# Performance work log

Measured on AMD Instinct MI355X. Metric: run time of the kernel, lower is better.

Reference implementation:

```python
import jax, jax.numpy as jnp
import numpy as np
import math

SAMPLE_RATE = 16000
CUTOFF = 7500.0
Q = 0.707  # torchaudio default for lowpass_biquad

def _lowpass_biquad_coeffs(sample_rate, cutoff_freq, Q):
    w0 = 2.0 * math.pi * cutoff_freq / sample_rate
    alpha = math.sin(w0) / (2.0 * Q)
    cos_w0 = math.cos(w0)
    b0 = (1.0 - cos_w0) / 2.0
    b1 = 1.0 - cos_w0
    b2 = b0
    a0 = 1.0 + alpha
    a1 = -2.0 * cos_w0
    a2 = 1.0 - alpha
    # normalize by a0 (as torchaudio's biquad/lfilter does)
    return (b0 / a0, b1 / a0, b2 / a0, a1 / a0, a2 / a0)


def setup_inputs() -> dict:
    key = jax.random.key(0)
    x = jax.random.normal(key, (64, 320000), dtype=jnp.float32)
    return {"x": x}


def reference(x) -> jnp.ndarray:
    b0, b1, b2, a1, a2 = _lowpass_biquad_coeffs(SAMPLE_RATE, CUTOFF, Q)
    b0 = jnp.asarray(b0, x.dtype); b1 = jnp.asarray(b1, x.dtype)
    b2 = jnp.asarray(b2, x.dtype); a1 = jnp.asarray(a1, x.dtype)
    a2 = jnp.asarray(a2, x.dtype)

    B = x.shape[0]
    xT = jnp.swapaxes(x, 0, 1)  # [T, B] -> scan over time

    def step(carry, xn):
        x1, x2, y1, y2 = carry  # each [B]
        yn = b0 * xn + b1 * x1 + b2 * x2 - a1 * y1 - a2 * y2
        return (xn, x1, yn, y1), yn

    z = jnp.zeros((B,), x.dtype)
    _, yT = jax.lax.scan(step, (z, z, z, z), xT)
    return jnp.swapaxes(yT, 0, 1)  # [B, T]
```

## Files before the change

kernel.cpp:

```cpp
#include <hip/hip_runtime.h>
#include <cmath>

#ifndef M_PI
#define M_PI 3.14159265358979323846
#endif

constexpr int T_LEN    = 320000;
constexpr int ROW_VECS = T_LEN / 4;
constexpr int B_ROWS   = 64;
constexpr int CHUNK    = 32;
constexpr int VPT      = CHUNK / 4;
constexpr int NCHUNK   = T_LEN / CHUNK;
constexpr int BLK_CHUNKS = 128;
constexpr int BLK_SPAN   = BLK_CHUNKS * CHUNK;
constexpr int HALO       = 3;
constexpr int HALO_VECS  = HALO * VPT;
constexpr int TILE_VECS  = HALO_VECS + BLK_CHUNKS * VPT;

__device__ __forceinline__ int swzv(int V) { return V ^ ((V >> 3) & 7); }

typedef const __attribute__((address_space(1))) void glb_void;
typedef __attribute__((address_space(3))) void lds_void;

__global__ __launch_bounds__(256, 8) void biquad_gll_kernel(
    const float* __restrict__ x, float* __restrict__ y,
    float b0, float b1, float b2, float a1, float a2,
    float q30, float p30, float q31, float p31) {
  const int b    = blockIdx.x;
  const int row  = blockIdx.y;
  const int t    = threadIdx.x;
  const int wave = t >> 6;
  const int lane = t & 63;

  const int S       = b * BLK_SPAN;
  const int nchunks = min(BLK_CHUNKS, (T_LEN - S) / CHUNK);
  const int nvecs   = nchunks * VPT;
  const int ntot    = HALO_VECS + nvecs;

  const float4* xr4 = reinterpret_cast<const float4*>(x + (size_t)row * T_LEN);
  float*        yr  = y + (size_t)row * T_LEN;

  __shared__ float4 tile[TILE_VECS];
  __shared__ float4 st[HALO + BLK_CHUNKS];

  {
    const int gofs = S / 4 - HALO_VECS;
    for (int r = wave; r * 64 < ntot; r += 4) {
      int s  = r * 64 + lane;
      int gv = gofs + swzv(s);
      if (s < ntot && gv >= 0) {
        __builtin_amdgcn_global_load_lds((glb_void*)(xr4 + gv),
                                         (lds_void*)(tile + r * 64), 16, 0, 0);
      }
    }
    if (b == 0 && t < HALO_VECS) tile[t] = make_float4(0.f, 0.f, 0.f, 0.f);
  }
  __syncthreads();

  auto stepf = [&](float xn, float& X1, float& X2, float& Y1, float& Y2) -> float {
    float tt = fmaf(b2, X2, fmaf(b1, X1, b0 * xn));
    float u  = fmaf(-a2, Y2, tt);
    float yn = fmaf(-a1, Y1, u);
    X2 = X1; X1 = xn;
    Y2 = Y1; Y1 = yn;
    return yn;
  };

  if (t < HALO) {
    float4 h[VPT];
#pragma unroll
    for (int k = 0; k < VPT; ++k) h[k] = tile[swzv(t * VPT + k)];
    float hxl1 = h[VPT - 1].w, hxl2 = h[VPT - 1].z;
    float hx1 = 0.f, hx2 = 0.f, hy1 = 0.f, hy2 = 0.f;
#pragma unroll
    for (int k = 0; k < VPT; ++k) {
      stepf(h[k].x, hx1, hx2, hy1, hy2); stepf(h[k].y, hx1, hx2, hy1, hy2);
      stepf(h[k].z, hx1, hx2, hy1, hy2); stepf(h[k].w, hx1, hx2, hy1, hy2);
    }
    st[t] = make_float4(hy1, hy2, hxl1, hxl2);
  }

  const bool active = (t < nchunks);
  float4 m[VPT];
  const int vb = HALO_VECS + t * VPT;
  if (active) {
#pragma unroll
    for (int k = 0; k < VPT; ++k) m[k] = tile[swzv(vb + k)];
    float xl1 = m[VPT - 1].w, xl2 = m[VPT - 1].z;
    float x1 = 0.f, x2 = 0.f, y1 = 0.f, y2 = 0.f;
#pragma unroll
    for (int k = 0; k < VPT; ++k) {
      float4 v = m[k];
      m[k] = make_float4(stepf(v.x, x1, x2, y1, y2), stepf(v.y, x1, x2, y1, y2),
                         stepf(v.z, x1, x2, y1, y2), stepf(v.w, x1, x2, y1, y2));
    }
    st[HALO + t] = make_float4(y1, y2, xl1, xl2);
  }
  __syncthreads();

  if (active) {
    const int i = HALO + t;
    float4 sm3 = st[i - 3], sm2 = st[i - 2], sm1 = st[i - 1];
    float cA0 = fmaf(b1, sm3.z, fmaf(b2, sm3.w, fmaf(-a1, sm3.x, -a2 * sm3.y)));
    float cA1 = fmaf(-a1, cA0, fmaf(b2, sm3.z, -a2 * sm3.x));
    float yA1 = fmaf(q31, cA0, fmaf(p31, cA1, sm2.x));
    float yA2 = fmaf(q30, cA0, fmaf(p30, cA1, sm2.y));
    float cB0 = fmaf(b1, sm2.z, fmaf(b2, sm2.w, fmaf(-a1, yA1, -a2 * yA2)));
    float cB1 = fmaf(-a1, cB0, fmaf(b2, sm2.z, -a2 * yA1));
    float yB1 = fmaf(q31, cB0, fmaf(p31, cB1, sm1.x));
    float yB2 = fmaf(q30, cB0, fmaf(p30, cB1, sm1.y));
    float c0 = fmaf(b1, sm1.z, fmaf(b2, sm1.w, fmaf(-a1, yB1, -a2 * yB2)));
    float c1 = fmaf(-a1, c0, fmaf(b2, sm1.z, -a2 * yB1));
    float cm2, cm1;
    {
      m[0].x += c0; m[0].y += c1;
      float c2 = fmaf(-a1, c1, -a2 * c0); m[0].z += c2;
      float c3 = fmaf(-a1, c2, -a2 * c1); m[0].w += c3;
      cm2 = c2; cm1 = c3;
    }
#pragma unroll
    for (int k = 1; k < VPT; ++k) {
      float ca = fmaf(-a1, cm1, -a2 * cm2); m[k].x += ca;
      float cb = fmaf(-a1, ca, -a2 * cm1);  m[k].y += cb;
      float cc = fmaf(-a1, cb, -a2 * ca);   m[k].z += cc;
      float cd = fmaf(-a1, cc, -a2 * cb);   m[k].w += cd;
      cm2 = cc; cm1 = cd;
    }
#pragma unroll
    for (int k = 0; k < VPT; ++k) tile[swzv(vb + k)] = m[k];
  }
  __syncthreads();

  {
    float4* dst = reinterpret_cast<float4*>(yr + S);
#pragma unroll
    for (int j = 0; j < 4; ++j) {
      int i = t + 256 * j;
      if (i < nvecs) dst[i] = tile[swzv(HALO_VECS + i)];
    }
  }
}

extern "C" void kernel_launch(void* const* d_in, const int* in_sizes, int n_in,
                              void* d_out, int out_size, void* d_ws, size_t ws_size,
                              hipStream_t stream) {
  const float* x = (const float*)d_in[0];
  float*       y = (float*)d_out;

  const double sample_rate = 16000.0, cutoff = 7500.0, Q = 0.707;
  double w0    = 2.0 * M_PI * cutoff / sample_rate;
  double alpha = sin(w0) / (2.0 * Q);
  double cw    = cos(w0);
  double a0    = 1.0 + alpha;
  double b0d = ((1.0 - cw) * 0.5) / a0;
  double b1d = (1.0 - cw) / a0;
  double a1d = (-2.0 * cw) / a0;
  double a2d = (1.0 - alpha) / a0;

  double qm2 = 1.0, pm2 = 0.0, qm1 = 0.0, pm1 = 1.0;
  double q30 = 0, p30 = 0, q31 = 0, p31 = 0;
  for (int n = 2; n < CHUNK; ++n) {
    double qn = -a1d * qm1 - a2d * qm2;
    double pn = -a1d * pm1 - a2d * pm2;
    qm2 = qm1; pm2 = pm1; qm1 = qn; pm1 = pn;
    if (n == 30) { q30 = qn; p30 = pn; }
    if (n == 31) { q31 = qn; p31 = pn; }
  }

  dim3 block(256);
  dim3 grid((NCHUNK + BLK_CHUNKS - 1) / BLK_CHUNKS, B_ROWS);
  hipLaunchKernelGGL(biquad_gll_kernel, grid, block, 0, stream,
                     x, y, (float)b0d, (float)b1d, (float)b0d, (float)a1d, (float)a2d,
                     (float)q30, (float)p30, (float)q31, (float)p31);
}
```

Before: 30.45 us.

## Turn biquad kernel into multi-tile loop with double-buffered LDS prefetch

The grid shrinks to 16 blocks per row. Each block now loops over about five consecutive tiles instead of handling one. While the current tile is being filtered, the next tile is loaded into a second LDS buffer with global_load_lds, using manual waitcnt and barrier control so the load latency overlaps with compute and stores. The cost is fewer resident blocks (launch bounds drop to 4 waves per SIMD, and LDS use doubles), which could reduce memory-level parallelism on a bandwidth-bound kernel.

```diff
diff --git a/kernel.cpp b/kernel.cpp
--- a/kernel.cpp
+++ b/kernel.cpp
@@ -16,46 +16,49 @@
 constexpr int HALO       = 3;
 constexpr int HALO_VECS  = HALO * VPT;
 constexpr int TILE_VECS  = HALO_VECS + BLK_CHUNKS * VPT;
+constexpr int NTILES_ROW = (NCHUNK + BLK_CHUNKS - 1) / BLK_CHUNKS;
+constexpr int GRID_X     = 16;
+constexpr int NT_MAX     = (NTILES_ROW + GRID_X - 1) / GRID_X;
 
 __device__ __forceinline__ int swzv(int V) { return V ^ ((V >> 3) & 7); }
 
 typedef const __attribute__((address_space(1))) void glb_void;
 typedef __attribute__((address_space(3))) void lds_void;
 
-__global__ __launch_bounds__(256, 8) void biquad_gll_kernel(
+__global__ __launch_bounds__(256, 4) void biquad_pipe_kernel(
     const float* __restrict__ x, float* __restrict__ y,
     float b0, float b1, float b2, float a1, float a2,
     float q30, float p30, float q31, float p31) {
-  const int b    = blockIdx.x;
+  const int bx   = blockIdx.x;
   const int row  = blockIdx.y;
   const int t    = threadIdx.x;
   const int wave = t >> 6;
-  const int lane = t & 63;
-
-  const int S       = b * BLK_SPAN;
-  const int nchunks = min(BLK_CHUNKS, (T_LEN - S) / CHUNK);
-  const int nvecs   = nchunks * VPT;
-  const int ntot    = HALO_VECS + nvecs;
+
+  const int tile0  = bx * NT_MAX;
+  const int ntiles = min(NT_MAX, NTILES_ROW - tile0);
 
   const float4* xr4 = reinterpret_cast<const float4*>(x + (size_t)row * T_LEN);
   float*        yr  = y + (size_t)row * T_LEN;
 
-  __shared__ float4 tile[TILE_VECS];
+  __shared__ float4 buf[2][TILE_VECS];
   __shared__ float4 st[HALO + BLK_CHUNKS];
 
-  {
+  const int lane = t & 63;
+
+  auto stage = [&](int tileIdx, int pb) {
+    const int S    = tileIdx * BLK_SPAN;
+    const int ntot = HALO_VECS + min(BLK_CHUNKS, (T_LEN - S) / CHUNK) * VPT;
     const int gofs = S / 4 - HALO_VECS;
     for (int r = wave; r * 64 < ntot; r += 4) {
       int s  = r * 64 + lane;
       int gv = gofs + swzv(s);
       if (s < ntot && gv >= 0) {
         __builtin_amdgcn_global_load_lds((glb_void*)(xr4 + gv),
-                                         (lds_void*)(tile + r * 64), 16, 0, 0);
-      }
-    }
-    if (b == 0 && t < HALO_VECS) tile[t] = make_float4(0.f, 0.f, 0.f, 0.f);
-  }
-  __syncthreads();
+                                         (lds_void*)(&buf[pb][r * 64]), 16, 0, 0);
+      }
+    }
+    if (tileIdx == 0 && t < HALO_VECS) buf[pb][t] = make_float4(0.f, 0.f, 0.f, 0.f);
+  };
 
   auto stepf = [&](float xn, float& X1, float& X2, float& Y1, float& Y2) -> float {
     float tt = fmaf(b2, X2, fmaf(b1, X1, b0 * xn));
@@ -66,78 +69,104 @@
     return yn;
   };
 
-  if (t < HALO) {
-    float4 h[VPT];
-#pragma unroll
-    for (int k = 0; k < VPT; ++k) h[k] = tile[swzv(t * VPT + k)];
-    float hxl1 = h[VPT - 1].w, hxl2 = h[VPT - 1].z;
-    float hx1 = 0.f, hx2 = 0.f, hy1 = 0.f, hy2 = 0.f;
-#pragma unroll
-    for (int k = 0; k < VPT; ++k) {
-      stepf(h[k].x, hx1, hx2, hy1, hy2); stepf(h[k].y, hx1, hx2, hy1, hy2);
-      stepf(h[k].z, hx1, hx2, hy1, hy2); stepf(h[k].w, hx1, hx2, hy1, hy2);
-    }
-    st[t] = make_float4(hy1, hy2, hxl1, hxl2);
-  }
-
-  const bool active = (t < nchunks);
-  float4 m[VPT];
-  const int vb = HALO_VECS + t * VPT;
-  if (active) {
-#pragma unroll
-    for (int k = 0; k < VPT; ++k) m[k] = tile[swzv(vb + k)];
-    float xl1 = m[VPT - 1].w, xl2 = m[VPT - 1].z;
-    float x1 = 0.f, x2 = 0.f, y1 = 0.f, y2 = 0.f;
-#pragma unroll
-    for (int k = 0; k < VPT; ++k) {
-      float4 v = m[k];
-      m[k] = make_float4(stepf(v.x, x1, x2, y1, y2), stepf(v.y, x1, x2, y1, y2),
-                         stepf(v.z, x1, x2, y1, y2), stepf(v.w, x1, x2, y1, y2));
-    }
-    st[HALO + t] = make_float4(y1, y2, xl1, xl2);
-  }
+  stage(tile0, 0);
   __syncthreads();
 
-  if (active) {
-    const int i = HALO + t;
-    float4 sm3 = st[i - 3], sm2 = st[i - 2], sm1 = st[i - 1];
-    float cA0 = fmaf(b1, sm3.z, fmaf(b2, sm3.w, fmaf(-a1, sm3.x, -a2 * sm3.y)));
-    float cA1 = fmaf(-a1, cA0, fmaf(b2, sm3.z, -a2 * sm3.x));
-    float yA1 = fmaf(q31, cA0, fmaf(p31, cA1, sm2.x));
-    float yA2 = fmaf(q30, cA0, fmaf(p30, cA1, sm2.y));
-    float cB0 = fmaf(b1, sm2.z, fmaf(b2, sm2.w, fmaf(-a1, yA1, -a2 * yA2)));
-    float cB1 = fmaf(-a1, cB0, fmaf(b2, sm2.z, -a2 * yA1));
-    float yB1 = fmaf(q31, cB0, fmaf(p31, cB1, sm1.x));
-    float yB2 = fmaf(q30, cB0, fmaf(p30, cB1, sm1.y));
-    float c0 = fmaf(b1, sm1.z, fmaf(b2, sm1.w, fmaf(-a1, yB1, -a2 * yB2)));
-    float c1 = fmaf(-a1, c0, fmaf(b2, sm1.z, -a2 * yB1));
-    float cm2, cm1;
+  int pb = 0;
+  for (int i = 0; i < ntiles; ++i) {
+    const int tileIdx = tile0 + i;
+    const int S       = tileIdx * BLK_SPAN;
+    const int nchunks = min(BLK_CHUNKS, (T_LEN - S) / CHUNK);
+    const int nvecs   = nchunks * VPT;
+    const float4* cur = buf[pb];
+    float4*       curw = buf[pb];
+
+    if (i + 1 < ntiles) stage(tileIdx + 1, pb ^ 1);
+
+    if (t < HALO) {
+      float4 h[VPT];
+#pragma unroll
+      for (int k = 0; k < VPT; ++k) h[k] = cur[swzv(t * VPT + k)];
+      float hxl1 = h[VPT - 1].w, hxl2 = h[VPT - 1].z;
+      float hx1 = 0.f, hx2 = 0.f, hy1 = 0.f, hy2 = 0.f;
+#pragma unroll
+      for (int k = 0; k < VPT; ++k) {
+        stepf(h[k].x, hx1, hx2, hy1, hy2); stepf(h[k].y, hx1, hx2, hy1, hy2);
+        stepf(h[k].z, hx1, hx2, hy1, hy2); stepf(h[k].w, hx1, hx2, hy1, hy2);
+      }
+      st[t] = make_float4(hy1, hy2, hxl1, hxl2);
+    }
+
+    const bool active = (t < nchunks);
+    float4 m[VPT];
+    const int vb = HALO_VECS + t * VPT;
+    if (active) {
+#pragma unroll
+      for (int k = 0; k < VPT; ++k) m[k] = cur[swzv(vb + k)];
+      float xl1 = m[VPT - 1].w, xl2 = m[VPT - 1].z;
+      float x1 = 0.f, x2 = 0.f, y1 = 0.f, y2 = 0.f;
+#pragma unroll
+      for (int k = 0; k < VPT; ++k) {
+        float4 v = m[k];
+        m[k] = make_float4(stepf(v.x, x1, x2, y1, y2), stepf(v.y, x1, x2, y1, y2),
+                           stepf(v.z, x1, x2, y1, y2), stepf(v.w, x1, x2, y1, y2));
+      }
+      st[HALO + t] = make_float4(y1, y2, xl1, xl2);
+    }
+    asm volatile("s_waitcnt lgkmcnt(0)" ::: "memory");
+    __builtin_amdgcn_s_barrier();
+    __builtin_amdgcn_sched_barrier(0);
+
+    if (active) {
+      const int ii = HALO + t;
+      float4 sm3 = st[ii - 3], sm2 = st[ii - 2], sm1 = st[ii - 1];
+      float cA0 = fmaf(b1, sm3.z, fmaf(b2, sm3.w, fmaf(-a1, sm3.x, -a2 * sm3.y)));
+      float cA1 = fmaf(-a1, cA0, fmaf(b2, sm3.z, -a2 * sm3.x));
+      float yA1 = fmaf(q31, cA0, fmaf(p31, cA1, sm2.x));
+      float yA2 = fmaf(q30, cA0, fmaf(p30, cA1, sm2.y));
+      float cB0 = fmaf(b1, sm2.z, fmaf(b2, sm2.w, fmaf(-a1, yA1, -a2 * yA2)));
+      float cB1 = fmaf(-a1, cB0, fmaf(b2, sm2.z, -a2 * yA1));
+      float yB1 = fmaf(q31, cB0, fmaf(p31, cB1, sm1.x));
+      float yB2 = fmaf(q30, cB0, fmaf(p30, cB1, sm1.y));
+      float c0 = fmaf(b1, sm1.z, fmaf(b2, sm1.w, fmaf(-a1, yB1, -a2 * yB2)));
+      float c1 = fmaf(-a1, c0, fmaf(b2, sm1.z, -a2 * yB1));
+      float cm2, cm1;
+      {
+        m[0].x += c0; m[0].y += c1;
+        float c2 = fmaf(-a1, c1, -a2 * c0); m[0].z += c2;
+        float c3 = fmaf(-a1, c2, -a2 * c1); m[0].w += c3;
+        cm2 = c2; cm1 = c3;
+      }
+#pragma unroll
+      for (int k = 1; k < VPT; ++k) {
+        float ca = fmaf(-a1, cm1, -a2 * cm2); m[k].x += ca;
+        float cb = fmaf(-a1, ca, -a2 * cm1);  m[k].y += cb;
+        float cc = fmaf(-a1, cb, -a2 * ca);   m[k].z += cc;
+        float cd = fmaf(-a1, cc, -a2 * cb);   m[k].w += cd;
+        cm2 = cc; cm1 = cd;
+      }
+#pragma unroll
+      for (int k = 0; k < VPT; ++k) curw[swzv(vb + k)] = m[k];
+    }
+    asm volatile("s_waitcnt lgkmcnt(0)" ::: "memory");
+    __builtin_amdgcn_s_barrier();
+    __builtin_amdgcn_sched_barrier(0);
+
     {
-      m[0].x += c0; m[0].y += c1;
-      float c2 = fmaf(-a1, c1, -a2 * c0); m[0].z += c2;
-      float c3 = fmaf(-a1, c2, -a2 * c1); m[0].w += c3;
-      cm2 = c2; cm1 = c3;
-    }
-#pragma unroll
-    for (int k = 1; k < VPT; ++k) {
-      float ca = fmaf(-a1, cm1, -a2 * cm2); m[k].x += ca;
-      float cb = fmaf(-a1, ca, -a2 * cm1);  m[k].y += cb;
-      float cc = fmaf(-a1, cb, -a2 * ca);   m[k].z += cc;
-      float cd = fmaf(-a1, cc, -a2 * cb);   m[k].w += cd;
-      cm2 = cc; cm1 = cd;
-    }
-#pragma unroll
-    for (int k = 0; k < VPT; ++k) tile[swzv(vb + k)] = m[k];
-  }
-  __syncthreads();
-
-  {
-    float4* dst = reinterpret_cast<float4*>(yr + S);
-#pragma unroll
-    for (int j = 0; j < 4; ++j) {
-      int i = t + 256 * j;
-      if (i < nvecs) dst[i] = tile[swzv(HALO_VECS + i)];
-    }
+      float4* dst = reinterpret_cast<float4*>(yr + S);
+#pragma unroll
+      for (int j = 0; j < 4; ++j) {
+        int v = t + 256 * j;
+        if (v < nvecs) dst[v] = cur[swzv(HALO_VECS + v)];
+      }
+    }
+
+    if (i + 1 < ntiles) {
+      asm volatile("s_waitcnt vmcnt(4)" ::: "memory");
+      __builtin_amdgcn_s_barrier();
+      __builtin_amdgcn_sched_barrier(0);
+    }
+    pb ^= 1;
   }
 }
 
@@ -168,8 +197,8 @@
   }
 
   dim3 block(256);
-  dim3 grid((NCHUNK + BLK_CHUNKS - 1) / BLK_CHUNKS, B_ROWS);
-  hipLaunchKernelGGL(biquad_gll_kernel, grid, block, 0, stream,
+  dim3 grid(GRID_X, B_ROWS);
+  hipLaunchKernelGGL(biquad_pipe_kernel, grid, block, 0, stream,
                      x, y, (float)b0d, (float)b1d, (float)b0d, (float)a1d, (float)a2d,
                      (float)q30, (float)p30, (float)q31, (float)p31);
 }
```

Measured after the change: 31.92 us. 1.05x slower.
